# Optimization experiments

Hardware: AMD Instinct MI355X
Metric: run time of the kernel (lower is better)

The kernel has to match this reference:

```python
import jax, jax.numpy as jnp
import numpy as np

D_MODEL = 1024
N_HEADS = 16
D_K = D_MODEL // N_HEADS
B, L = 8, 512


def setup_inputs() -> dict:
    key = jax.random.key(0)
    ks = jax.random.split(key, 12)
    s = 0.02
    return {
        "q": jax.random.normal(ks[0], (B, L, D_MODEL), jnp.float32),
        "k": jax.random.normal(ks[1], (B, L, D_MODEL), jnp.float32),
        "v": jax.random.normal(ks[2], (B, L, D_MODEL), jnp.float32),
        "rel_pos_emb": jax.random.normal(ks[3], (L, L, D_MODEL), jnp.float32) * s,
        "mask": jnp.ones((1, 1, L, L), jnp.int32),
        "Wq": jax.random.normal(ks[4], (D_MODEL, D_MODEL), jnp.float32) * s,
        "bq": jnp.zeros((D_MODEL,), jnp.float32),
        "Wk": jax.random.normal(ks[5], (D_MODEL, D_MODEL), jnp.float32) * s,
        "bk": jnp.zeros((D_MODEL,), jnp.float32),
        "Wv": jax.random.normal(ks[6], (D_MODEL, D_MODEL), jnp.float32) * s,
        "bv": jnp.zeros((D_MODEL,), jnp.float32),
        "Wo": jax.random.normal(ks[7], (D_MODEL, D_MODEL), jnp.float32) * s,
        "bo": jnp.zeros((D_MODEL,), jnp.float32),
    }


def reference(q, k, v, rel_pos_emb, mask, Wq, bq, Wk, bk, Wv, bv, Wo, bo):
    Bn, Ln, D = q.shape
    H, dk = N_HEADS, D // N_HEADS
    # QKV projections (nn.Linear: x @ W^T + b), split heads -> [B,H,L,dk]
    qh = (q @ Wq.T + bq).reshape(Bn, Ln, H, dk).transpose(0, 2, 1, 3)
    kh = (k @ Wk.T + bk).reshape(Bn, Ln, H, dk).transpose(0, 2, 1, 3)
    vh = (v @ Wv.T + bv).reshape(Bn, Ln, H, dk).transpose(0, 2, 1, 3)
    # relative position embeddings -> [H,L,L,dk]
    rel = rel_pos_emb.reshape(Ln, Ln, H, dk).transpose(2, 0, 1, 3)
    scale = 1.0 / jnp.sqrt(jnp.float32(dk))
    scores = jnp.einsum('bhld,bhrd->bhlr', qh, kh) * scale
    scores = scores + jnp.einsum('bhld,hlrd->bhlr', qh, rel)
    scores = jnp.where(mask == 0, jnp.float32(-1e9), scores)
    attn = jax.nn.softmax(scores, axis=-1)  # dropout omitted (eval mode)
    out = jnp.einsum('bhlr,bhrd->bhld', attn, vh)
    out = out.transpose(0, 2, 1, 3).reshape(Bn, Ln, D)
    return out @ Wo.T + bo
```

## Files before the change

kernel.cpp:

```cpp
#include <hip/hip_runtime.h>

typedef __attribute__((ext_vector_type(8))) short short8;
typedef __attribute__((ext_vector_type(4))) float f32x4;
typedef __attribute__((ext_vector_type(4))) unsigned short u16x4;
typedef unsigned int u32;
typedef unsigned short ushort_t;

union frag_u { u32 w[4]; short8 s; };

static __device__ __forceinline__ unsigned short f2bf(float x) {
  union { float f; unsigned u; } v; v.f = x;
  unsigned r = v.u + 0x7fffu + ((v.u >> 16) & 1u);
  return (unsigned short)(r >> 16);
}
static __device__ __forceinline__ float bf2f(unsigned short h) {
  union { unsigned u; float f; } v; v.u = ((unsigned)h) << 16;
  return v.f;
}
static __device__ __forceinline__ u32 pk_bf16(float a, float b) {
  u32 r;
  asm("v_cvt_pk_bf16_f32 %0, %1, %2" : "=v"(r) : "v"(a), "v"(b));
  return r;
}

static __device__ __forceinline__ void gl_lds16(const void* g, void* s) {
  __builtin_amdgcn_global_load_lds(
      (const __attribute__((address_space(1))) void*)g,
      (__attribute__((address_space(3))) void*)s, 16, 0, 0);
}

__global__ __launch_bounds__(256) void to_bf16(const float* __restrict__ src,
                                               ushort_t* __restrict__ dst, int n4) {
  int i = blockIdx.x * blockDim.x + threadIdx.x;
  int stride = gridDim.x * blockDim.x;
  for (; i < n4; i += stride) {
    float4 x = *(const float4*)&src[i * 4];
    u16x4 o;
    o.x = f2bf(x.x); o.y = f2bf(x.y); o.z = f2bf(x.z); o.w = f2bf(x.w);
    *(u16x4*)&dst[i * 4] = o;
  }
}

__global__ __launch_bounds__(256) void split3_bf16(const float* __restrict__ src,
                                                   ushort_t* __restrict__ dst, int n) {
  int i = blockIdx.x * blockDim.x + threadIdx.x;
  int stride = gridDim.x * blockDim.x;
  for (; i < n; i += stride) {
    int r = i >> 10, c = i & 1023;
    float x = src[i];
    unsigned short hi = f2bf(x);
    unsigned short lo = f2bf(x - bf2f(hi));
    ushort_t* row = dst + (size_t)r * 3072;
    row[c] = hi; row[1024 + c] = hi; row[2048 + c] = lo;
  }
}

__global__ __launch_bounds__(256) void gemm_bf16(const ushort_t* __restrict__ A, int lda,
                                                 const ushort_t* __restrict__ Bw, int ldb,
                                                 const float* __restrict__ bias,
                                                 float* __restrict__ Cout, int K, int mode) {
  __shared__ ushort_t As[2][128 * 32];
  __shared__ ushort_t Bs[2][128 * 32];
  const int t = threadIdx.x;
  const int lane = t & 63;
  const int w = t >> 6;
  const int wr = w >> 1, wc = w & 1;
  const int mt = blockIdx.x >> 3, nt = blockIdx.x & 7;
  const int m0 = mt * 128, n0 = nt * 128;
  const int r16 = lane & 15, kb = lane >> 4;

  f32x4 acc[4][4];
#pragma unroll
  for (int mi = 0; mi < 4; ++mi)
#pragma unroll
    for (int ni = 0; ni < 4; ++ni) acc[mi][ni] = (f32x4){0.f, 0.f, 0.f, 0.f};

  auto STAGE = [&](int buf, int k0) {
#pragma unroll
    for (int i = 0; i < 2; ++i) {
      int c = i * 256 + t;
      int row = c >> 2, kc = (c & 3) * 8;
      gl_lds16(&A[(size_t)(m0 + row) * lda + k0 + kc], &As[buf][c * 8]);
      gl_lds16(&Bw[(size_t)(n0 + row) * ldb + k0 + kc], &Bs[buf][c * 8]);
    }
  };

  const int NT = K / 32;
  STAGE(0, 0);
  __syncthreads();
  int cur = 0;
  for (int kt = 0; kt < NT; ++kt) {
    if (kt + 1 < NT) STAGE(cur ^ 1, (kt + 1) * 32);
    short8 af[4], bf[4];
#pragma unroll
    for (int mi = 0; mi < 4; ++mi)
      af[mi] = *(const short8*)&As[cur][(wr * 64 + mi * 16 + r16) * 32 + kb * 8];
#pragma unroll
    for (int ni = 0; ni < 4; ++ni)
      bf[ni] = *(const short8*)&Bs[cur][(wc * 64 + ni * 16 + r16) * 32 + kb * 8];
#pragma unroll
    for (int mi = 0; mi < 4; ++mi)
#pragma unroll
      for (int ni = 0; ni < 4; ++ni)
        acc[mi][ni] = __builtin_amdgcn_mfma_f32_16x16x32_bf16(af[mi], bf[ni], acc[mi][ni], 0, 0, 0);
    __syncthreads();
    cur ^= 1;
  }

  const int rowD = (lane >> 4) * 4;
#pragma unroll
  for (int mi = 0; mi < 4; ++mi) {
#pragma unroll
    for (int ni = 0; ni < 4; ++ni) {
      int n = n0 + wc * 64 + ni * 16 + (lane & 15);
      float bv = bias[n];
      int mbase = m0 + wr * 64 + mi * 16 + rowD;
      float vals[4];
#pragma unroll
      for (int j = 0; j < 4; ++j) vals[j] = acc[mi][ni][j] + bv;
      if (mode == 0) {
#pragma unroll
        for (int j = 0; j < 4; ++j) {
          int m = mbase + j;
          int b = m >> 9, l = m & 511, hh = n >> 6, d = n & 63;
          Cout[(((size_t)(b * 16 + hh)) * 512 + l) * 64 + d] = vals[j];
        }
      } else if (mode == 1) {
#pragma unroll
        for (int j = 0; j < 4; ++j)
          Cout[(size_t)(mbase + j) * 1024 + n] = vals[j];
      } else if (mode == 2) {
        ushort_t* co = (ushort_t*)Cout;
#pragma unroll
        for (int j = 0; j < 4; ++j) {
          int m = mbase + j;
          int b = m >> 9, r = m & 511, hh = n >> 6, d = n & 63;
          co[(((size_t)(b * 16 + hh)) * 512 + r) * 64 + d] = f2bf(vals[j]);
        }
      } else {
        ushort_t* co = (ushort_t*)Cout;
        int b = mbase >> 9, r = mbase & 511, hh = n >> 6, d = n & 63;
        u16x4 pkv;
        pkv.x = f2bf(vals[0]); pkv.y = f2bf(vals[1]);
        pkv.z = f2bf(vals[2]); pkv.w = f2bf(vals[3]);
        *(u16x4*)&co[(((size_t)(b * 16 + hh)) * 64 + d) * 512 + r] = pkv;
      }
    }
  }
}

__global__ __launch_bounds__(256, 2) void attn_mfma(
    const float* __restrict__ qh, const ushort_t* __restrict__ khb,
    const ushort_t* __restrict__ vT, const float* __restrict__ rel,
    const int* __restrict__ mask, ushort_t* __restrict__ Abig) {
  __shared__ ushort_t qs[8][16][64];
  __shared__ float sp2[2][8][16][20];
  const int t = threadIdx.x;
  const int w = t >> 6, lane = t & 63, lh = lane & 15, lg = lane >> 4;
  const int bid = blockIdx.x;
  const int slot = bid & 7, grp = bid >> 3;
  const int h = slot * 2 + (grp & 1);
  const int l0 = (grp >> 1) * 16;
  const int b0 = w * 2;

  {
    int idx = t * 32;
    int b = idx >> 10, l = (idx >> 6) & 15, d0 = idx & 63;
    const float* src = &qh[(((size_t)(b * 16 + h)) * 512 + l0 + l) * 64 + d0];
    ushort_t* dst = &qs[b][l][d0];
#pragma unroll
    for (int j = 0; j < 8; ++j) {
      f32x4 xv = *(const f32x4*)&src[j * 4];
      u32 w0 = pk_bf16(xv[0], xv[1]), w1 = pk_bf16(xv[2], xv[3]);
      *(u32*)&dst[j * 4] = w0;
      *(u32*)&dst[j * 4 + 2] = w1;
    }
  }

  f32x4 R[16];
  auto LOAD_REL = [&](int r0_) {
#pragma unroll
    for (int li = 0; li < 4; ++li) {
      const float* rp = &rel[((size_t)(l0 + w * 4 + li) * 512 + r0_ + lh) * 1024 + h * 64 + lg * 8];
#pragma unroll
      for (int kb = 0; kb < 2; ++kb) {
        R[li * 4 + kb * 2 + 0] = *(const f32x4*)&rp[kb * 32];
        R[li * 4 + kb * 2 + 1] = *(const f32x4*)&rp[kb * 32 + 4];
      }
    }
  };
  LOAD_REL(0);

  f32x4 O[2][4];
#pragma unroll
  for (int i = 0; i < 2; ++i)
#pragma unroll
    for (int j = 0; j < 4; ++j) O[i][j] = (f32x4){0.f, 0.f, 0.f, 0.f};
  float m_run[2] = {-1e30f, -1e30f}, s_run[2] = {0.f, 0.f};

  __syncthreads();

  for (int it = 0; it < 32; ++it) {
    const int r0 = it * 16;
    const int cur = it & 1;

    short8 kf[2][2], vf[2][4];
#pragma unroll
    for (int bh = 0; bh < 2; ++bh) {
#pragma unroll
      for (int kb = 0; kb < 2; ++kb)
        kf[bh][kb] = *(const short8*)&khb[(((size_t)((b0 + bh) * 16 + h)) * 512 + r0 + lh) * 64 + kb * 32 + lg * 8];
#pragma unroll
      for (int dt = 0; dt < 4; ++dt)
        vf[bh][dt] = *(const short8*)&vT[(((size_t)((b0 + bh) * 16 + h)) * 64 + dt * 16 + lh) * 512 + r0 + lg * 8];
    }
    int4 mk = *(const int4*)&mask[(size_t)(l0 + lh) * 512 + r0 + lg * 4];

#pragma unroll
    for (int li = 0; li < 4; ++li) {
      frag_u a0, a1;
      f32x4 v00 = R[li * 4 + 0], v01 = R[li * 4 + 1];
      f32x4 v10 = R[li * 4 + 2], v11 = R[li * 4 + 3];
      a0.w[0] = pk_bf16(v00[0], v00[1]); a0.w[1] = pk_bf16(v00[2], v00[3]);
      a0.w[2] = pk_bf16(v01[0], v01[1]); a0.w[3] = pk_bf16(v01[2], v01[3]);
      a1.w[0] = pk_bf16(v10[0], v10[1]); a1.w[1] = pk_bf16(v10[2], v10[3]);
      a1.w[2] = pk_bf16(v11[0], v11[1]); a1.w[3] = pk_bf16(v11[2], v11[3]);
      short8 q0 = *(const short8*)&qs[lh & 7][w * 4 + li][lg * 8];
      short8 q1 = *(const short8*)&qs[lh & 7][w * 4 + li][32 + lg * 8];
      f32x4 acc = (f32x4){0.f, 0.f, 0.f, 0.f};
      acc = __builtin_amdgcn_mfma_f32_16x16x32_bf16(a0.s, q0, acc, 0, 0, 0);
      acc = __builtin_amdgcn_mfma_f32_16x16x32_bf16(a1.s, q1, acc, 0, 0, 0);
      if (lh < 8) *(f32x4*)&sp2[cur][lh][w * 4 + li][lg * 4] = acc;
    }
    if (it < 31) LOAD_REL(r0 + 16);
    __syncthreads();

#pragma unroll
    for (int bh = 0; bh < 2; ++bh) {
      short8 qb0 = *(const short8*)&qs[b0 + bh][lh][lg * 8];
      short8 qb1 = *(const short8*)&qs[b0 + bh][lh][32 + lg * 8];
      f32x4 s1 = (f32x4){0.f, 0.f, 0.f, 0.f};
      s1 = __builtin_amdgcn_mfma_f32_16x16x32_bf16(kf[bh][0], qb0, s1, 0, 0, 0);
      s1 = __builtin_amdgcn_mfma_f32_16x16x32_bf16(kf[bh][1], qb1, s1, 0, 0, 0);
      f32x4 s2 = *(const f32x4*)&sp2[cur][b0 + bh][lh][lg * 4];
      f32x4 S;
      S[0] = (mk.x == 0) ? -1e9f : (s1[0] * 0.125f + s2[0]);
      S[1] = (mk.y == 0) ? -1e9f : (s1[1] * 0.125f + s2[1]);
      S[2] = (mk.z == 0) ? -1e9f : (s1[2] * 0.125f + s2[2]);
      S[3] = (mk.w == 0) ? -1e9f : (s1[3] * 0.125f + s2[3]);
      float mt = fmaxf(fmaxf(S[0], S[1]), fmaxf(S[2], S[3]));
      mt = fmaxf(mt, __shfl_xor(mt, 16));
      mt = fmaxf(mt, __shfl_xor(mt, 32));
      float mn = fmaxf(m_run[bh], mt);
      float fsc = __expf(m_run[bh] - mn);
      f32x4 P;
      P[0] = __expf(S[0] - mn); P[1] = __expf(S[1] - mn);
      P[2] = __expf(S[2] - mn); P[3] = __expf(S[3] - mn);
      float ps = P[0] + P[1] + P[2] + P[3];
      ps += __shfl_xor(ps, 16);
      ps += __shfl_xor(ps, 32);
      s_run[bh] = s_run[bh] * fsc + ps;
      m_run[bh] = mn;
#pragma unroll
      for (int dt = 0; dt < 4; ++dt) O[bh][dt] *= fsc;
      u32 pk0 = pk_bf16(P[0], P[1]), pk1 = pk_bf16(P[2], P[3]);
      int s0l = (lh + 32 * lg) & 63;
      u32 w0 = (u32)__shfl((int)pk0, s0l), w1 = (u32)__shfl((int)pk1, s0l);
      u32 w2 = (u32)__shfl((int)pk0, s0l + 16), w3 = (u32)__shfl((int)pk1, s0l + 16);
      bool vld = (lg < 2);
      frag_u pb;
      pb.w[0] = vld ? w0 : 0u; pb.w[1] = vld ? w1 : 0u;
      pb.w[2] = vld ? w2 : 0u; pb.w[3] = vld ? w3 : 0u;
#pragma unroll
      for (int dt = 0; dt < 4; ++dt)
        O[bh][dt] = __builtin_amdgcn_mfma_f32_16x16x32_bf16(vf[bh][dt], pb.s, O[bh][dt], 0, 0, 0);
    }
  }

#pragma unroll
  for (int bh = 0; bh < 2; ++bh) {
    float inv = 1.0f / s_run[bh];
    ushort_t* rowp = &Abig[(size_t)((b0 + bh) * 512 + l0 + lh) * 3072];
#pragma unroll
    for (int dt = 0; dt < 4; ++dt) {
      int c = h * 64 + dt * 16 + lg * 4;
      f32x4 o = O[bh][dt];
      float x0 = o[0] * inv, x1 = o[1] * inv, x2 = o[2] * inv, x3 = o[3] * inv;
      u16x4 hi, lo;
      hi.x = f2bf(x0); lo.x = f2bf(x0 - bf2f(hi.x));
      hi.y = f2bf(x1); lo.y = f2bf(x1 - bf2f(hi.y));
      hi.z = f2bf(x2); lo.z = f2bf(x2 - bf2f(hi.z));
      hi.w = f2bf(x3); lo.w = f2bf(x3 - bf2f(hi.w));
      *(u16x4*)&rowp[c] = hi;
      *(u16x4*)&rowp[1024 + c] = lo;
      *(u16x4*)&rowp[2048 + c] = hi;
    }
  }
}

extern "C" void kernel_launch(void* const* d_in, const int* in_sizes, int n_in,
                              void* d_out, int out_size, void* d_ws, size_t ws_size,
                              hipStream_t stream) {
  const float* q    = (const float*)d_in[0];
  const float* k    = (const float*)d_in[1];
  const float* v    = (const float*)d_in[2];
  const float* rel  = (const float*)d_in[3];
  const int*   mask = (const int*)d_in[4];
  const float* Wq   = (const float*)d_in[5];
  const float* bq   = (const float*)d_in[6];
  const float* Wk   = (const float*)d_in[7];
  const float* bk   = (const float*)d_in[8];
  const float* Wv   = (const float*)d_in[9];
  const float* bv   = (const float*)d_in[10];
  const float* Wo   = (const float*)d_in[11];
  const float* bo   = (const float*)d_in[12];
  float* out = (float*)d_out;

  char* ws = (char*)d_ws;
  float*    qh  = (float*)(ws);
  ushort_t* khb = (ushort_t*)(ws + 16777216);
  ushort_t* vT  = (ushort_t*)(ws + 16777216 + 8388608);
  ushort_t* X   = (ushort_t*)(ws + 33554432);
  ushort_t* Y   = (ushort_t*)(ws + 58720256);
  ushort_t* qbf = X;
  ushort_t* kbf = X + 4194304;
  ushort_t* vbf = X + 8388608;
  ushort_t* Wqb = Y;
  ushort_t* Wkb = Y + 1048576;
  ushort_t* Wvb = Y + 2097152;

  to_bf16<<<1024, 256, 0, stream>>>(q, qbf, 1048576);
  to_bf16<<<1024, 256, 0, stream>>>(k, kbf, 1048576);
  to_bf16<<<1024, 256, 0, stream>>>(v, vbf, 1048576);
  to_bf16<<<256, 256, 0, stream>>>(Wq, Wqb, 262144);
  to_bf16<<<256, 256, 0, stream>>>(Wk, Wkb, 262144);
  to_bf16<<<256, 256, 0, stream>>>(Wv, Wvb, 262144);

  gemm_bf16<<<256, 256, 0, stream>>>(qbf, 1024, Wqb, 1024, bq, qh, 1024, 0);
  gemm_bf16<<<256, 256, 0, stream>>>(kbf, 1024, Wkb, 1024, bk, (float*)khb, 1024, 2);
  gemm_bf16<<<256, 256, 0, stream>>>(vbf, 1024, Wvb, 1024, bv, (float*)vT, 1024, 3);

  split3_bf16<<<1024, 256, 0, stream>>>(Wo, Y, 1048576);

  attn_mfma<<<512, 256, 0, stream>>>(qh, khb, vT, rel, mask, X);

  gemm_bf16<<<256, 256, 0, stream>>>(X, 3072, Y, 3072, bo, out, 3072, 1);
}
```

Measured before the change: 462.1 us.

## Merge QKV GEMMs into one launch, swizzle q LDS tile, pad score buffer

Combines the three Q/K/V projection GEMMs into a single 768-block launch. Each block picks its input, weight and output layout from its block index, which fills the GPU better and removes two launches. In the attention kernel, the bf16 q tile in LDS gets an XOR swizzle and the score scratch buffer gets a padded row dimension, both to reduce bank conflicts. The softmax/PV section is also wrapped in s_setprio. The output GEMM is specialised with constant strides.

```diff
diff --git a/kernel.cpp b/kernel.cpp
--- a/kernel.cpp
+++ b/kernel.cpp
@@ -55,10 +55,106 @@
   }
 }
 
-__global__ __launch_bounds__(256) void gemm_bf16(const ushort_t* __restrict__ A, int lda,
-                                                 const ushort_t* __restrict__ Bw, int ldb,
-                                                 const float* __restrict__ bias,
-                                                 float* __restrict__ Cout, int K, int mode) {
+__global__ __launch_bounds__(256) void gemm_qkv(
+    const ushort_t* __restrict__ qbf, const ushort_t* __restrict__ kbf,
+    const ushort_t* __restrict__ vbf, const ushort_t* __restrict__ Wqb,
+    const ushort_t* __restrict__ Wkb, const ushort_t* __restrict__ Wvb,
+    const float* __restrict__ bq, const float* __restrict__ bk,
+    const float* __restrict__ bv, float* __restrict__ qh,
+    ushort_t* __restrict__ khb, ushort_t* __restrict__ vT) {
+  __shared__ ushort_t As[2][128 * 32];
+  __shared__ ushort_t Bs[2][128 * 32];
+  const int t = threadIdx.x;
+  const int lane = t & 63;
+  const int w = t >> 6;
+  const int wr = w >> 1, wc = w & 1;
+  const int bid = blockIdx.x;
+  const int mt = bid / 24, ntg = bid % 24;
+  const int which = ntg >> 3, nt = ntg & 7;
+  const ushort_t* A  = which == 0 ? qbf : which == 1 ? kbf : vbf;
+  const ushort_t* Bw = which == 0 ? Wqb : which == 1 ? Wkb : Wvb;
+  const float* bias  = which == 0 ? bq  : which == 1 ? bk  : bv;
+  const int m0 = mt * 128, n0 = nt * 128;
+  const int r16 = lane & 15, kb = lane >> 4;
+
+  f32x4 acc[4][4];
+#pragma unroll
+  for (int mi = 0; mi < 4; ++mi)
+#pragma unroll
+    for (int ni = 0; ni < 4; ++ni) acc[mi][ni] = (f32x4){0.f, 0.f, 0.f, 0.f};
+
+  auto STAGE = [&](int buf, int k0) {
+#pragma unroll
+    for (int i = 0; i < 2; ++i) {
+      int c = i * 256 + t;
+      int row = c >> 2, kc = (c & 3) * 8;
+      gl_lds16(&A[(size_t)(m0 + row) * 1024 + k0 + kc], &As[buf][c * 8]);
+      gl_lds16(&Bw[(size_t)(n0 + row) * 1024 + k0 + kc], &Bs[buf][c * 8]);
+    }
+  };
+
+  STAGE(0, 0);
+  __syncthreads();
+  int cur = 0;
+  for (int kt = 0; kt < 32; ++kt) {
+    if (kt + 1 < 32) STAGE(cur ^ 1, (kt + 1) * 32);
+    short8 af[4], bf[4];
+#pragma unroll
+    for (int mi = 0; mi < 4; ++mi)
+      af[mi] = *(const short8*)&As[cur][(wr * 64 + mi * 16 + r16) * 32 + kb * 8];
+#pragma unroll
+    for (int ni = 0; ni < 4; ++ni)
+      bf[ni] = *(const short8*)&Bs[cur][(wc * 64 + ni * 16 + r16) * 32 + kb * 8];
+#pragma unroll
+    for (int mi = 0; mi < 4; ++mi)
+#pragma unroll
+      for (int ni = 0; ni < 4; ++ni)
+        acc[mi][ni] = __builtin_amdgcn_mfma_f32_16x16x32_bf16(af[mi], bf[ni], acc[mi][ni], 0, 0, 0);
+    __syncthreads();
+    cur ^= 1;
+  }
+
+  const int rowD = (lane >> 4) * 4;
+#pragma unroll
+  for (int mi = 0; mi < 4; ++mi) {
+#pragma unroll
+    for (int ni = 0; ni < 4; ++ni) {
+      int n = n0 + wc * 64 + ni * 16 + (lane & 15);
+      float bv4 = bias[n];
+      int mbase = m0 + wr * 64 + mi * 16 + rowD;
+      float vals[4];
+#pragma unroll
+      for (int j = 0; j < 4; ++j) vals[j] = acc[mi][ni][j] + bv4;
+      int hh = n >> 6, d = n & 63;
+      if (which == 0) {
+#pragma unroll
+        for (int j = 0; j < 4; ++j) {
+          int m = mbase + j;
+          int b = m >> 9, l = m & 511;
+          qh[(((size_t)(b * 16 + hh)) * 512 + l) * 64 + d] = vals[j];
+        }
+      } else if (which == 1) {
+#pragma unroll
+        for (int j = 0; j < 4; ++j) {
+          int m = mbase + j;
+          int b = m >> 9, r = m & 511;
+          khb[(((size_t)(b * 16 + hh)) * 512 + r) * 64 + d] = f2bf(vals[j]);
+        }
+      } else {
+        int b = mbase >> 9, r = mbase & 511;
+        u16x4 pkv;
+        pkv.x = f2bf(vals[0]); pkv.y = f2bf(vals[1]);
+        pkv.z = f2bf(vals[2]); pkv.w = f2bf(vals[3]);
+        *(u16x4*)&vT[(((size_t)(b * 16 + hh)) * 64 + d) * 512 + r] = pkv;
+      }
+    }
+  }
+}
+
+__global__ __launch_bounds__(256) void gemm_out(const ushort_t* __restrict__ A,
+                                                const ushort_t* __restrict__ Bw,
+                                                const float* __restrict__ bias,
+                                                float* __restrict__ Cout) {
   __shared__ ushort_t As[2][128 * 32];
   __shared__ ushort_t Bs[2][128 * 32];
   const int t = threadIdx.x;
@@ -80,17 +176,16 @@
     for (int i = 0; i < 2; ++i) {
       int c = i * 256 + t;
       int row = c >> 2, kc = (c & 3) * 8;
-      gl_lds16(&A[(size_t)(m0 + row) * lda + k0 + kc], &As[buf][c * 8]);
-      gl_lds16(&Bw[(size_t)(n0 + row) * ldb + k0 + kc], &Bs[buf][c * 8]);
+      gl_lds16(&A[(size_t)(m0 + row) * 3072 + k0 + kc], &As[buf][c * 8]);
+      gl_lds16(&Bw[(size_t)(n0 + row) * 3072 + k0 + kc], &Bs[buf][c * 8]);
     }
   };
 
-  const int NT = K / 32;
   STAGE(0, 0);
   __syncthreads();
   int cur = 0;
-  for (int kt = 0; kt < NT; ++kt) {
-    if (kt + 1 < NT) STAGE(cur ^ 1, (kt + 1) * 32);
+  for (int kt = 0; kt < 96; ++kt) {
+    if (kt + 1 < 96) STAGE(cur ^ 1, (kt + 1) * 32);
     short8 af[4], bf[4];
 #pragma unroll
     for (int mi = 0; mi < 4; ++mi)
@@ -115,36 +210,9 @@
       int n = n0 + wc * 64 + ni * 16 + (lane & 15);
       float bv = bias[n];
       int mbase = m0 + wr * 64 + mi * 16 + rowD;
-      float vals[4];
-#pragma unroll
-      for (int j = 0; j < 4; ++j) vals[j] = acc[mi][ni][j] + bv;
-      if (mode == 0) {
-#pragma unroll
-        for (int j = 0; j < 4; ++j) {
-          int m = mbase + j;
-          int b = m >> 9, l = m & 511, hh = n >> 6, d = n & 63;
-          Cout[(((size_t)(b * 16 + hh)) * 512 + l) * 64 + d] = vals[j];
-        }
-      } else if (mode == 1) {
-#pragma unroll
-        for (int j = 0; j < 4; ++j)
-          Cout[(size_t)(mbase + j) * 1024 + n] = vals[j];
-      } else if (mode == 2) {
-        ushort_t* co = (ushort_t*)Cout;
-#pragma unroll
-        for (int j = 0; j < 4; ++j) {
-          int m = mbase + j;
-          int b = m >> 9, r = m & 511, hh = n >> 6, d = n & 63;
-          co[(((size_t)(b * 16 + hh)) * 512 + r) * 64 + d] = f2bf(vals[j]);
-        }
-      } else {
-        ushort_t* co = (ushort_t*)Cout;
-        int b = mbase >> 9, r = mbase & 511, hh = n >> 6, d = n & 63;
-        u16x4 pkv;
-        pkv.x = f2bf(vals[0]); pkv.y = f2bf(vals[1]);
-        pkv.z = f2bf(vals[2]); pkv.w = f2bf(vals[3]);
-        *(u16x4*)&co[(((size_t)(b * 16 + hh)) * 64 + d) * 512 + r] = pkv;
-      }
+#pragma unroll
+      for (int j = 0; j < 4; ++j)
+        Cout[(size_t)(mbase + j) * 1024 + n] = acc[mi][ni][j] + bv;
     }
   }
 }
@@ -154,7 +222,7 @@
     const ushort_t* __restrict__ vT, const float* __restrict__ rel,
     const int* __restrict__ mask, ushort_t* __restrict__ Abig) {
   __shared__ ushort_t qs[8][16][64];
-  __shared__ float sp2[2][8][16][20];
+  __shared__ float sp2[2][8][17][20];
   const int t = threadIdx.x;
   const int w = t >> 6, lane = t & 63, lh = lane & 15, lg = lane >> 4;
   const int bid = blockIdx.x;
@@ -167,13 +235,16 @@
     int idx = t * 32;
     int b = idx >> 10, l = (idx >> 6) & 15, d0 = idx & 63;
     const float* src = &qh[(((size_t)(b * 16 + h)) * 512 + l0 + l) * 64 + d0];
-    ushort_t* dst = &qs[b][l][d0];
-#pragma unroll
-    for (int j = 0; j < 8; ++j) {
-      f32x4 xv = *(const f32x4*)&src[j * 4];
-      u32 w0 = pk_bf16(xv[0], xv[1]), w1 = pk_bf16(xv[2], xv[3]);
-      *(u32*)&dst[j * 4] = w0;
-      *(u32*)&dst[j * 4 + 2] = w1;
+    int xr = (l & 7) ^ b;
+#pragma unroll
+    for (int jj = 0; jj < 4; ++jj) {
+      f32x4 x0 = *(const f32x4*)&src[jj * 8];
+      f32x4 x1 = *(const f32x4*)&src[jj * 8 + 4];
+      frag_u fu;
+      fu.w[0] = pk_bf16(x0[0], x0[1]); fu.w[1] = pk_bf16(x0[2], x0[3]);
+      fu.w[2] = pk_bf16(x1[0], x1[1]); fu.w[3] = pk_bf16(x1[2], x1[3]);
+      int pos = ((d0 >> 3) + jj) ^ xr;
+      *(short8*)&qs[b][l][pos * 8] = fu.s;
     }
   }
 
@@ -225,20 +296,24 @@
       a0.w[2] = pk_bf16(v01[0], v01[1]); a0.w[3] = pk_bf16(v01[2], v01[3]);
       a1.w[0] = pk_bf16(v10[0], v10[1]); a1.w[1] = pk_bf16(v10[2], v10[3]);
       a1.w[2] = pk_bf16(v11[0], v11[1]); a1.w[3] = pk_bf16(v11[2], v11[3]);
-      short8 q0 = *(const short8*)&qs[lh & 7][w * 4 + li][lg * 8];
-      short8 q1 = *(const short8*)&qs[lh & 7][w * 4 + li][32 + lg * 8];
+      int l = w * 4 + li;
+      int xr2 = (l & 7) ^ (lh & 7);
+      short8 q0 = *(const short8*)&qs[lh & 7][l][(lg ^ xr2) * 8];
+      short8 q1 = *(const short8*)&qs[lh & 7][l][((4 + lg) ^ xr2) * 8];
       f32x4 acc = (f32x4){0.f, 0.f, 0.f, 0.f};
       acc = __builtin_amdgcn_mfma_f32_16x16x32_bf16(a0.s, q0, acc, 0, 0, 0);
       acc = __builtin_amdgcn_mfma_f32_16x16x32_bf16(a1.s, q1, acc, 0, 0, 0);
-      if (lh < 8) *(f32x4*)&sp2[cur][lh][w * 4 + li][lg * 4] = acc;
+      if (lh < 8) *(f32x4*)&sp2[cur][lh][l][lg * 4] = acc;
     }
     if (it < 31) LOAD_REL(r0 + 16);
     __syncthreads();
 
+    __builtin_amdgcn_s_setprio(1);
 #pragma unroll
     for (int bh = 0; bh < 2; ++bh) {
-      short8 qb0 = *(const short8*)&qs[b0 + bh][lh][lg * 8];
-      short8 qb1 = *(const short8*)&qs[b0 + bh][lh][32 + lg * 8];
+      int xqk = (lh & 7) ^ (b0 + bh);
+      short8 qb0 = *(const short8*)&qs[b0 + bh][lh][(lg ^ xqk) * 8];
+      short8 qb1 = *(const short8*)&qs[b0 + bh][lh][((4 + lg) ^ xqk) * 8];
       f32x4 s1 = (f32x4){0.f, 0.f, 0.f, 0.f};
       s1 = __builtin_amdgcn_mfma_f32_16x16x32_bf16(kf[bh][0], qb0, s1, 0, 0, 0);
       s1 = __builtin_amdgcn_mfma_f32_16x16x32_bf16(kf[bh][1], qb1, s1, 0, 0, 0);
@@ -275,6 +350,7 @@
       for (int dt = 0; dt < 4; ++dt)
         O[bh][dt] = __builtin_amdgcn_mfma_f32_16x16x32_bf16(vf[bh][dt], pb.s, O[bh][dt], 0, 0, 0);
     }
+    __builtin_amdgcn_s_setprio(0);
   }
 
 #pragma unroll
@@ -336,13 +412,12 @@
   to_bf16<<<256, 256, 0, stream>>>(Wk, Wkb, 262144);
   to_bf16<<<256, 256, 0, stream>>>(Wv, Wvb, 262144);
 
-  gemm_bf16<<<256, 256, 0, stream>>>(qbf, 1024, Wqb, 1024, bq, qh, 1024, 0);
-  gemm_bf16<<<256, 256, 0, stream>>>(kbf, 1024, Wkb, 1024, bk, (float*)khb, 1024, 2);
-  gemm_bf16<<<256, 256, 0, stream>>>(vbf, 1024, Wvb, 1024, bv, (float*)vT, 1024, 3);
+  gemm_qkv<<<768, 256, 0, stream>>>(qbf, kbf, vbf, Wqb, Wkb, Wvb,
+                                    bq, bk, bv, qh, khb, vT);
 
   split3_bf16<<<1024, 256, 0, stream>>>(Wo, Y, 1048576);
 
   attn_mfma<<<512, 256, 0, stream>>>(qh, khb, vT, rel, mask, X);
 
-  gemm_bf16<<<256, 256, 0, stream>>>(X, 3072, Y, 3072, bo, out, 3072, 1);
-}
+  gemm_out<<<256, 256, 0, stream>>>(X, Y, bo, out);
+}
```

Result: faster. 438.8 us (-5.0%).
